# Optimization experiments

Measured on AMD Instinct MI355X. Metric: run time of the kernel, lower is better.

Reference implementation:

```python
import jax, jax.numpy as jnp
import numpy as np

D_MODEL = 1024
H = 16
DK = D_MODEL // H
B, S = 2, 2048
NEG = -1e9


def setup_inputs() -> dict:
    key = jax.random.key(0)
    ks = jax.random.split(key, 7)
    scale = 1.0 / np.sqrt(D_MODEL)
    inp = {
        "q": jax.random.normal(ks[0], (B, S, D_MODEL), jnp.float32),
        "k": jax.random.normal(ks[1], (B, S, D_MODEL), jnp.float32),
        "v": jax.random.normal(ks[2], (B, S, D_MODEL), jnp.float32),
        # causal mask, broadcastable to (B, H, S, S); positions with 0 are masked
        "mask": jnp.tril(jnp.ones((S, S), dtype=bool))[None, None, :, :],
        "w_q": jax.random.normal(ks[3], (D_MODEL, D_MODEL), jnp.float32) * scale,
        "w_k": jax.random.normal(ks[4], (D_MODEL, D_MODEL), jnp.float32) * scale,
        "w_v": jax.random.normal(ks[5], (D_MODEL, D_MODEL), jnp.float32) * scale,
        "w_o": jax.random.normal(ks[6], (D_MODEL, D_MODEL), jnp.float32) * scale,
    }
    return inp


def reference(q, k, v, mask, w_q, w_k, w_v, w_o):
    # Linear projections (nn.Linear with bias=False: x @ W.T)
    query = q @ w_q.T  # (B, S, d_model)
    key_ = k @ w_k.T
    value = v @ w_v.T
    # split heads -> (B, h, S, dk)
    def split(x):
        return x.reshape(x.shape[0], x.shape[1], H, DK).transpose(0, 2, 1, 3)
    qh, kh, vh = split(query), split(key_), split(value)
    # scaled dot-product attention with full score materialization
    scores = jnp.einsum("bhqd,bhkd->bhqk", qh, kh) / jnp.sqrt(jnp.float32(DK))
    scores = jnp.where(mask, scores, NEG)
    attn = jax.nn.softmax(scores, axis=-1)  # (B, h, S, S); dropout p=0.0 -> identity
    out = jnp.einsum("bhqk,bhkd->bhqd", attn, vh)
    # merge heads -> (B, S, d_model)
    out = out.transpose(0, 2, 1, 3).reshape(out.shape[0], -1, H * DK)
    return out @ w_o.T
```

## Files before the change

kernel.cpp:

```cpp
#include <hip/hip_runtime.h>
#include <cstdint>
#include <cstddef>

typedef __bf16 bf16;
typedef __attribute__((ext_vector_type(4))) __bf16 bf16x4;
typedef __attribute__((ext_vector_type(8))) __bf16 bf16x8;
typedef __attribute__((ext_vector_type(4))) float floatx4;
typedef __attribute__((ext_vector_type(4))) short short4v;

#define MFMA16(a, b, c) __builtin_amdgcn_mfma_f32_16x16x32_bf16((a), (b), (c), 0, 0, 0)

__device__ __forceinline__ floatx4 MFMAK16(bf16x4 a, bf16x4 b, floatx4 c) {
#if __has_builtin(__builtin_amdgcn_mfma_f32_16x16x16bf16_1k)
  return __builtin_amdgcn_mfma_f32_16x16x16bf16_1k(
      __builtin_bit_cast(short4v, a), __builtin_bit_cast(short4v, b), c, 0, 0, 0);
#else
  floatx4 d;
  asm("v_mfma_f32_16x16x16_bf16 %0, %1, %2, %3"
      : "=v"(d)
      : "v"(a), "v"(b), "v"(c));
  return d;
#endif
}

constexpr int DMODEL = 1024;
constexpr int NH = 16;
constexpr int DKH = 64;
constexpr int B_ = 2;
constexpr int S_ = 2048;
constexpr int MTOT = B_ * S_;
constexpr float CEXP = 0.125f * 1.44269504f;

__device__ __forceinline__ void load_lds16(const void* g, void* l) {
  __builtin_amdgcn_global_load_lds(
      (const __attribute__((address_space(1))) uint32_t*)g,
      (__attribute__((address_space(3))) uint32_t*)l, 16, 0, 0);
}

__device__ __forceinline__ bf16x8 frag64(const bf16* lds, int row, int p) {
  int s = p ^ (row & 7);
  return *(const bf16x8*)&lds[row * 64 + s * 8];
}
__device__ __forceinline__ bf16x4 frag64h(const bf16* lds, int row, int p, int h) {
  int s = p ^ (row & 7);
  return *(const bf16x4*)&lds[row * 64 + s * 8 + h * 4];
}

__device__ __forceinline__ void stage32_bf16(const bf16* __restrict__ src,
                                             bf16* lds, int wave, int lane,
                                             int ldg) {
#pragma unroll
  for (int i = 0; i < 2; ++i) {
    int cb = (wave * 2 + i) * 64;
    int c = cb + lane;
    int r = c >> 2;
    int s = (c & 3) ^ ((r >> 1) & 3);
    load_lds16(&src[(size_t)r * ldg + s * 8], &lds[cb * 8]);
  }
}
__device__ __forceinline__ bf16x8 frag32_bf16(const bf16* lds, int row,
                                              int quad) {
  int s = quad ^ ((row >> 1) & 3);
  return *(const bf16x8*)&lds[row * 32 + s * 8];
}
__device__ __forceinline__ void stage32_f32(const float* __restrict__ src,
                                            float* lds, int wave, int lane,
                                            int ldg) {
#pragma unroll
  for (int i = 0; i < 4; ++i) {
    int cb = (wave * 4 + i) * 64;
    int c = cb + lane;
    int r = c >> 3;
    int s = (c & 7) ^ (r & 7);
    load_lds16(&src[(size_t)r * ldg + s * 4], &lds[cb * 4]);
  }
}
__device__ __forceinline__ bf16x8 frag32_f32(const float* lds, int row,
                                             int quad) {
  int s1 = (2 * quad) ^ (row & 7);
  int s2 = (2 * quad + 1) ^ (row & 7);
  float4 a = *(const float4*)&lds[row * 32 + s1 * 4];
  float4 b = *(const float4*)&lds[row * 32 + s2 * 4];
  bf16x8 h = {(bf16)a.x, (bf16)a.y, (bf16)a.z, (bf16)a.w,
              (bf16)b.x, (bf16)b.y, (bf16)b.z, (bf16)b.w};
  return h;
}

__global__ __launch_bounds__(256) void convert_kernel(
    const float* __restrict__ q, const float* __restrict__ k,
    const float* __restrict__ v, const float* __restrict__ wq,
    const float* __restrict__ wk, const float* __restrict__ wv,
    const float* __restrict__ wo, bf16* __restrict__ qb, bf16* __restrict__ kb,
    bf16* __restrict__ vb, bf16* __restrict__ wqb, bf16* __restrict__ wkb,
    bf16* __restrict__ wvb, bf16* __restrict__ wob) {
  const float* src;
  bf16* dst;
  size_t n;
  switch (blockIdx.y) {
    case 0: src = q;  dst = qb;  n = (size_t)MTOT * DMODEL; break;
    case 1: src = k;  dst = kb;  n = (size_t)MTOT * DMODEL; break;
    case 2: src = v;  dst = vb;  n = (size_t)MTOT * DMODEL; break;
    case 3: src = wq; dst = wqb; n = (size_t)DMODEL * DMODEL; break;
    case 4: src = wk; dst = wkb; n = (size_t)DMODEL * DMODEL; break;
    case 5: src = wv; dst = wvb; n = (size_t)DMODEL * DMODEL; break;
    default: src = wo; dst = wob; n = (size_t)DMODEL * DMODEL; break;
  }
  size_t idx = ((size_t)blockIdx.x * 256 + threadIdx.x) * 8;
  if (idx >= n) return;
  float4 f0 = *(const float4*)&src[idx];
  float4 f1 = *(const float4*)&src[idx + 4];
  bf16x8 h = {(bf16)f0.x, (bf16)f0.y, (bf16)f0.z, (bf16)f0.w,
              (bf16)f1.x, (bf16)f1.y, (bf16)f1.z, (bf16)f1.w};
  *(bf16x8*)&dst[idx] = h;
}

template <typename TC>
__device__ __forceinline__ void gemm64(const bf16* __restrict__ A,
                                       const bf16* __restrict__ W,
                                       TC* __restrict__ C,
                                       bf16* __restrict__ vt, int K,
                                       int m0, int n0, float ascale) {
  constexpr int N = DMODEL;
  __shared__ alignas(16) bf16 As[128 * 64];
  __shared__ alignas(16) bf16 Bs[128 * 64];

  const int tid = threadIdx.x;
  const int wave = tid >> 6;
  const int lane = tid & 63;
  const int quad = lane >> 4;
  const int l16 = lane & 15;
  const int wm = (wave >> 1) * 64;
  const int wn = (wave & 1) * 64;

  floatx4 acc[4][4] = {};

  for (int k0 = 0; k0 < K; k0 += 64) {
#pragma unroll
    for (int i = 0; i < 4; ++i) {
      int cb = (wave * 4 + i) * 64;
      int c = cb + lane;
      int r = c >> 3;
      int s = (c & 7) ^ (r & 7);
      load_lds16(&A[(size_t)(m0 + r) * K + k0 + s * 8], &As[cb * 8]);
      load_lds16(&W[(size_t)(n0 + r) * K + k0 + s * 8], &Bs[cb * 8]);
    }
    __syncthreads();

#pragma unroll
    for (int kk = 0; kk < 2; ++kk) {
      bf16x8 af[4], bfv[4];
#pragma unroll
      for (int mi = 0; mi < 4; ++mi)
        af[mi] = frag64(As, wm + mi * 16 + l16, kk * 4 + quad);
#pragma unroll
      for (int ni = 0; ni < 4; ++ni)
        bfv[ni] = frag64(Bs, wn + ni * 16 + l16, kk * 4 + quad);
#pragma unroll
      for (int mi = 0; mi < 4; ++mi)
#pragma unroll
        for (int ni = 0; ni < 4; ++ni)
          acc[mi][ni] = MFMA16(af[mi], bfv[ni], acc[mi][ni]);
    }
    __syncthreads();
  }

  if (vt) {
#pragma unroll
    for (int mi = 0; mi < 4; ++mi)
#pragma unroll
      for (int ni = 0; ni < 4; ++ni)
#pragma unroll
        for (int r = 0; r < 4; ++r) {
          int row = m0 + wm + mi * 16 + quad * 4 + r;
          int col = n0 + wn + ni * 16 + l16;
          int bb = row >> 11, s = row & 2047;
          int h = col >> 6, d = col & 63;
          vt[(size_t)((bb * NH + h) * DKH + d) * S_ + s] = (bf16)acc[mi][ni][r];
        }
  } else {
#pragma unroll
    for (int mi = 0; mi < 4; ++mi)
#pragma unroll
      for (int ni = 0; ni < 4; ++ni)
#pragma unroll
        for (int r = 0; r < 4; ++r) {
          int row = m0 + wm + mi * 16 + quad * 4 + r;
          int col = n0 + wn + ni * 16 + l16;
          C[(size_t)row * N + col] = (TC)(acc[mi][ni][r] * ascale);
        }
  }
}

__global__ __launch_bounds__(256, 3) void qkv64_kernel(
    const bf16* __restrict__ q, const bf16* __restrict__ k,
    const bf16* __restrict__ v, const bf16* __restrict__ wq,
    const bf16* __restrict__ wk, const bf16* __restrict__ wv,
    bf16* __restrict__ Q, bf16* __restrict__ K, bf16* __restrict__ Vt) {
  const int bid = blockIdx.x;
  const int xcd = bid & 7;
  const int j = bid >> 3;
  const int n = j & 7;
  const int rowslot = j >> 3;
  const int p = xcd * 12 + rowslot;
  const int z = p >> 5;
  const int y = p & 31;

  const bf16* A = (z == 0) ? q : (z == 1) ? k : v;
  const bf16* W = (z == 0) ? wq : (z == 1) ? wk : wv;
  bf16* C = (z == 0) ? Q : K;
  gemm64<bf16>(A, W, (z == 2) ? nullptr : C, (z == 2) ? Vt : nullptr,
               DMODEL, y * 128, n * 128, (z == 0) ? CEXP : 1.0f);
}

__global__ __launch_bounds__(256) void oproj64_kernel(
    const bf16* __restrict__ A, const bf16* __restrict__ W,
    float* __restrict__ C) {
  constexpr int K = DMODEL;
  constexpr int N = DMODEL;
  __shared__ alignas(16) bf16 As[64 * 64];
  __shared__ alignas(16) bf16 Bs[128 * 64];

  const int bid = blockIdx.x;
  const int xcd = bid & 7;
  const int j = bid >> 3;
  const int n = j & 7;
  const int slot = j >> 3;
  const int mt = xcd * 8 + slot;
  const int m0 = mt * 64;
  const int n0 = n * 128;

  const int tid = threadIdx.x;
  const int wave = tid >> 6;
  const int lane = tid & 63;
  const int quad = lane >> 4;
  const int l16 = lane & 15;
  const int wm = (wave >> 1) * 32;
  const int wn = (wave & 1) * 64;

  floatx4 acc[2][4] = {};

  for (int k0 = 0; k0 < K; k0 += 64) {
#pragma unroll
    for (int i = 0; i < 2; ++i) {
      int cb = (wave * 2 + i) * 64;
      int c = cb + lane;
      int r = c >> 3;
      int s = (c & 7) ^ (r & 7);
      load_lds16(&A[(size_t)(m0 + r) * K + k0 + s * 8], &As[cb * 8]);
    }
#pragma unroll
    for (int i = 0; i < 4; ++i) {
      int cb = (wave * 4 + i) * 64;
      int c = cb + lane;
      int r = c >> 3;
      int s = (c & 7) ^ (r & 7);
      load_lds16(&W[(size_t)(n0 + r) * K + k0 + s * 8], &Bs[cb * 8]);
    }
    __syncthreads();

#pragma unroll
    for (int kk = 0; kk < 2; ++kk) {
      bf16x8 af[2], bfv[4];
#pragma unroll
      for (int mi = 0; mi < 2; ++mi)
        af[mi] = frag64(As, wm + mi * 16 + l16, kk * 4 + quad);
#pragma unroll
      for (int ni = 0; ni < 4; ++ni)
        bfv[ni] = frag64(Bs, wn + ni * 16 + l16, kk * 4 + quad);
#pragma unroll
      for (int mi = 0; mi < 2; ++mi)
#pragma unroll
        for (int ni = 0; ni < 4; ++ni)
          acc[mi][ni] = MFMA16(af[mi], bfv[ni], acc[mi][ni]);
    }
    __syncthreads();
  }

#pragma unroll
  for (int mi = 0; mi < 2; ++mi)
#pragma unroll
    for (int ni = 0; ni < 4; ++ni)
#pragma unroll
      for (int r = 0; r < 4; ++r) {
        int row = m0 + wm + mi * 16 + quad * 4 + r;
        int col = n0 + wn + ni * 16 + l16;
        C[(size_t)row * N + col] = acc[mi][ni][r];
      }
}

template <typename TA, typename TW, typename TC>
__device__ __forceinline__ void gemm_core(const TA* __restrict__ A,
                                          const TW* __restrict__ W,
                                          TC* __restrict__ C,
                                          bf16* __restrict__ vt, int K,
                                          int m0, int n0, float ascale) {
  constexpr int N = DMODEL;
  __shared__ alignas(16) char smem[128 * 32 * (sizeof(TA) + sizeof(TW))];
  TA* As = (TA*)smem;
  TW* Bs = (TW*)(smem + 128 * 32 * sizeof(TA));

  const int tid = threadIdx.x;
  const int wave = tid >> 6;
  const int lane = tid & 63;
  const int quad = lane >> 4;
  const int l16 = lane & 15;
  const int wm = (wave >> 1) * 64;
  const int wn = (wave & 1) * 64;

  floatx4 acc[4][4] = {};

  for (int k0 = 0; k0 < K; k0 += 32) {
    if constexpr (sizeof(TA) == 2)
      stage32_bf16((const bf16*)A + (size_t)m0 * K + k0, (bf16*)As, wave, lane, K);
    else
      stage32_f32((const float*)A + (size_t)m0 * K + k0, (float*)As, wave, lane, K);
    if constexpr (sizeof(TW) == 2)
      stage32_bf16((const bf16*)W + (size_t)n0 * K + k0, (bf16*)Bs, wave, lane, K);
    else
      stage32_f32((const float*)W + (size_t)n0 * K + k0, (float*)Bs, wave, lane, K);
    __syncthreads();

    bf16x8 af[4], bfv[4];
#pragma unroll
    for (int mi = 0; mi < 4; ++mi) {
      if constexpr (sizeof(TA) == 2)
        af[mi] = frag32_bf16((const bf16*)As, wm + mi * 16 + l16, quad);
      else
        af[mi] = frag32_f32((const float*)As, wm + mi * 16 + l16, quad);
    }
#pragma unroll
    for (int ni = 0; ni < 4; ++ni) {
      if constexpr (sizeof(TW) == 2)
        bfv[ni] = frag32_bf16((const bf16*)Bs, wn + ni * 16 + l16, quad);
      else
        bfv[ni] = frag32_f32((const float*)Bs, wn + ni * 16 + l16, quad);
    }
#pragma unroll
    for (int mi = 0; mi < 4; ++mi)
#pragma unroll
      for (int ni = 0; ni < 4; ++ni)
        acc[mi][ni] = MFMA16(af[mi], bfv[ni], acc[mi][ni]);
    __syncthreads();
  }

  if (vt) {
#pragma unroll
    for (int mi = 0; mi < 4; ++mi)
#pragma unroll
      for (int ni = 0; ni < 4; ++ni)
#pragma unroll
        for (int r = 0; r < 4; ++r) {
          int row = m0 + wm + mi * 16 + quad * 4 + r;
          int col = n0 + wn + ni * 16 + l16;
          int bb = row >> 11, s = row & 2047;
          int h = col >> 6, d = col & 63;
          vt[(size_t)((bb * NH + h) * DKH + d) * S_ + s] = (bf16)acc[mi][ni][r];
        }
  } else {
#pragma unroll
    for (int mi = 0; mi < 4; ++mi)
#pragma unroll
      for (int ni = 0; ni < 4; ++ni)
#pragma unroll
        for (int r = 0; r < 4; ++r) {
          int row = m0 + wm + mi * 16 + quad * 4 + r;
          int col = n0 + wn + ni * 16 + l16;
          C[(size_t)row * N + col] = (TC)(acc[mi][ni][r] * ascale);
        }
  }
}

__global__ __launch_bounds__(256) void qkv_f32_kernel(
    const float* __restrict__ q, const float* __restrict__ k,
    const float* __restrict__ v, const float* __restrict__ wq,
    const float* __restrict__ wk, const float* __restrict__ wv,
    bf16* __restrict__ Q, bf16* __restrict__ K, bf16* __restrict__ Vt) {
  const int bid = blockIdx.x;
  const int xcd = bid & 7;
  const int j = bid >> 3;
  const int n = j & 7;
  const int rowslot = j >> 3;
  const int p = xcd * 12 + rowslot;
  const int z = p >> 5;
  const int y = p & 31;
  const float* A = (z == 0) ? q : (z == 1) ? k : v;
  const float* W = (z == 0) ? wq : (z == 1) ? wk : wv;
  bf16* C = (z == 0) ? Q : K;
  gemm_core<float, float, bf16>(A, W, (z == 2) ? nullptr : C,
                                (z == 2) ? Vt : nullptr, DMODEL, y * 128,
                                n * 128, (z == 0) ? CEXP : 1.0f);
}

__global__ __launch_bounds__(256) void oproj_f32_kernel(
    const bf16* __restrict__ A, const float* __restrict__ W,
    float* __restrict__ C) {
  const int bid = blockIdx.x;
  const int xcd = bid & 7;
  const int j = bid >> 3;
  const int n = j & 7;
  const int rowslot = j >> 3;
  const int y = xcd * 4 + rowslot;
  gemm_core<bf16, float, float>(A, W, C, nullptr, DMODEL, y * 128, n * 128,
                                1.0f);
}

__device__ __forceinline__ void stage_kv(const bf16* __restrict__ K,
                                         const bf16* __restrict__ Vt,
                                         bf16* Ks, bf16* Vts, size_t baseQ,
                                         size_t baseV, int kt, int wave,
                                         int lane) {
#pragma unroll
  for (int i = 0; i < 2; ++i) {
    int cb = (wave * 2 + i) * 64;
    int c = cb + lane;
    int r = c >> 3;
    int s = (c & 7) ^ (r & 7);
    load_lds16(&K[baseQ + (size_t)(kt * 64 + r) * DMODEL + s * 8], &Ks[cb * 8]);
    load_lds16(&Vt[baseV + (size_t)r * S_ + kt * 64 + s * 8], &Vts[cb * 8]);
  }
}

template <bool DIAG>
__device__ __forceinline__ void attn_tile(const bf16* Ks, const bf16* Vts,
                                          const bf16x8 qf[2], floatx4 ot[4],
                                          float lp[4], int quad, int l16,
                                          int qb) {
  floatx4 sa[4] = {};
#pragma unroll
  for (int kk = 0; kk < 2; ++kk)
#pragma unroll
    for (int kg = 0; kg < 4; ++kg) {
      bf16x8 ka = frag64(Ks, kg * 16 + l16, kk * 4 + quad);
      sa[kg] = MFMA16(ka, qf[kk], sa[kg]);
    }

  bf16x4 pb[4];
#pragma unroll
  for (int kg = 0; kg < 4; ++kg) {
    float pv[4];
#pragma unroll
    for (int r = 0; r < 4; ++r) {
      float s = sa[kg][r];
      if (DIAG) {
        int key = kg * 16 + quad * 4 + r;
        s = (key > qb) ? -3.0e38f : s;
      }
      float p = __builtin_amdgcn_exp2f(s);
      lp[kg] += p;
      pv[r] = p;
    }
    pb[kg] = bf16x4{(bf16)pv[0], (bf16)pv[1], (bf16)pv[2], (bf16)pv[3]};
  }

#pragma unroll
  for (int kg = 0; kg < 4; ++kg)
#pragma unroll
    for (int di = 0; di < 4; ++di) {
      bf16x4 va = frag64h(Vts, di * 16 + l16, kg * 2 + (quad >> 1), quad & 1);
      ot[di] = MFMAK16(va, pb[kg], ot[di]);
    }
}

__global__ __launch_bounds__(256) void attn7_kernel(const bf16* __restrict__ Q,
                                                    const bf16* __restrict__ K,
                                                    const bf16* __restrict__ Vt,
                                                    bf16* __restrict__ O) {
  __shared__ alignas(16) bf16 Ks[2][64 * 64];
  __shared__ alignas(16) bf16 Vts[2][64 * 64];

  const int tid = threadIdx.x;
  const int wave = tid >> 6;
  const int lane = tid & 63;
  const int quad = lane >> 4;
  const int l16 = lane & 15;

  const int j = blockIdx.x;
  const int bh = j & 31;
  const int pr = j >> 5;
  const int qtL = pr;
  const int qtH = 31 - pr;
  const int h = bh & 15;
  const int b = bh >> 4;
  const size_t baseQ = (size_t)b * S_ * DMODEL + (size_t)h * DKH;
  const size_t baseV = (size_t)bh * DKH * S_;

  bf16x8 qfL[2], qfH[2];
#pragma unroll
  for (int kk = 0; kk < 2; ++kk) {
    qfL[kk] = *(const bf16x8*)&Q[baseQ +
        (size_t)(qtL * 64 + wave * 16 + l16) * DMODEL + kk * 32 + quad * 8];
    qfH[kk] = *(const bf16x8*)&Q[baseQ +
        (size_t)(qtH * 64 + wave * 16 + l16) * DMODEL + kk * 32 + quad * 8];
  }

  floatx4 otL[4] = {}, otH[4] = {};
  float lpL[4] = {}, lpH[4] = {};
  const int qb = wave * 16 + l16;

  stage_kv(K, Vt, Ks[0], Vts[0], baseQ, baseV, 0, wave, lane);
  __syncthreads();

  for (int kt = 0; kt < qtH; ++kt) {
    const int cur = kt & 1;
    stage_kv(K, Vt, Ks[cur ^ 1], Vts[cur ^ 1], baseQ, baseV, kt + 1, wave, lane);

    __builtin_amdgcn_s_setprio(1);
    if (kt < qtL)
      attn_tile<false>(Ks[cur], Vts[cur], qfL, otL, lpL, quad, l16, qb);
    else if (kt == qtL)
      attn_tile<true>(Ks[cur], Vts[cur], qfL, otL, lpL, quad, l16, qb);
    attn_tile<false>(Ks[cur], Vts[cur], qfH, otH, lpH, quad, l16, qb);
    __builtin_amdgcn_s_setprio(0);

    __syncthreads();
  }
  {
    const int cur = qtH & 1;
    attn_tile<true>(Ks[cur], Vts[cur], qfH, otH, lpH, quad, l16, qb);
  }

  float lL = (lpL[0] + lpL[1]) + (lpL[2] + lpL[3]);
  lL += __shfl_xor(lL, 16, 64);
  lL += __shfl_xor(lL, 32, 64);
  float lH = (lpH[0] + lpH[1]) + (lpH[2] + lpH[3]);
  lH += __shfl_xor(lH, 16, 64);
  lH += __shfl_xor(lH, 32, 64);
  const float invL = 1.0f / lL;
  const float invH = 1.0f / lH;

  const size_t orowL = baseQ + (size_t)(qtL * 64 + wave * 16 + l16) * DMODEL;
  const size_t orowH = baseQ + (size_t)(qtH * 64 + wave * 16 + l16) * DMODEL;
#pragma unroll
  for (int di = 0; di < 4; ++di)
#pragma unroll
    for (int r = 0; r < 4; ++r) {
      O[orowL + di * 16 + quad * 4 + r] = (bf16)(otL[di][r] * invL);
      O[orowH + di * 16 + quad * 4 + r] = (bf16)(otH[di][r] * invH);
    }
}

extern "C" void kernel_launch(void* const* d_in, const int* in_sizes, int n_in,
                              void* d_out, int out_size, void* d_ws,
                              size_t ws_size, hipStream_t stream) {
  const float* q = (const float*)d_in[0];
  const float* k = (const float*)d_in[1];
  const float* v = (const float*)d_in[2];
  const float* wq = (const float*)d_in[4];
  const float* wk = (const float*)d_in[5];
  const float* wv = (const float*)d_in[6];
  const float* wo = (const float*)d_in[7];
  float* out = (float*)d_out;

  const size_t MB = 1024 * 1024;
  char* base = (char*)d_ws;
  bf16* Qp = (bf16*)(base);
  bf16* Kp = (bf16*)(base + 8 * MB);
  bf16* VtG = (bf16*)(base + 16 * MB);
  bf16* AO = (bf16*)(base + 24 * MB);

  if (ws_size >= 64 * MB) {
    bf16* qb = (bf16*)(base + 32 * MB);
    bf16* kb = (bf16*)(base + 40 * MB);
    bf16* vb = (bf16*)(base + 48 * MB);
    bf16* wqb = (bf16*)(base + 56 * MB);
    bf16* wkb = (bf16*)(base + 58 * MB);
    bf16* wvb = (bf16*)(base + 60 * MB);
    bf16* wob = (bf16*)(base + 62 * MB);
    convert_kernel<<<dim3(2048, 7), 256, 0, stream>>>(
        q, k, v, wq, wk, wv, wo, qb, kb, vb, wqb, wkb, wvb, wob);
    qkv64_kernel<<<dim3(768), 256, 0, stream>>>(
        qb, kb, vb, wqb, wkb, wvb, Qp, Kp, VtG);
    attn7_kernel<<<dim3(512), 256, 0, stream>>>(Qp, Kp, VtG, AO);
    oproj64_kernel<<<dim3(512), 256, 0, stream>>>(AO, wob, out);
  } else {
    qkv_f32_kernel<<<dim3(768), 256, 0, stream>>>(
        q, k, v, wq, wk, wv, Qp, Kp, VtG);
    attn7_kernel<<<dim3(512), 256, 0, stream>>>(Qp, Kp, VtG, AO);
    oproj_f32_kernel<<<dim3(256), 256, 0, stream>>>(AO, wo, out);
  }
}
```

Measured before the change: 208.2 us.

## Use two waves of 32 query rows with register-cached K/V fragments

The attention kernel now runs 128 threads per block, and each wave handles 32 query rows instead of 16. K and V fragments are loaded from LDS into registers once per key tile and reused across both 16-row query groups, which halves the LDS fragment reads per query row. Each wave now stages more of the K/V tile. The cost is higher register pressure and fewer waves resident per CU, which reduces latency hiding.

```diff
diff --git a/kernel.cpp b/kernel.cpp
--- a/kernel.cpp
+++ b/kernel.cpp
@@ -404,14 +404,14 @@
                                 1.0f);
 }
 
-__device__ __forceinline__ void stage_kv(const bf16* __restrict__ K,
-                                         const bf16* __restrict__ Vt,
-                                         bf16* Ks, bf16* Vts, size_t baseQ,
-                                         size_t baseV, int kt, int wave,
-                                         int lane) {
-#pragma unroll
-  for (int i = 0; i < 2; ++i) {
-    int cb = (wave * 2 + i) * 64;
+__device__ __forceinline__ void stage_kv2(const bf16* __restrict__ K,
+                                          const bf16* __restrict__ Vt,
+                                          bf16* Ks, bf16* Vts, size_t baseQ,
+                                          size_t baseV, int kt, int wave,
+                                          int lane) {
+#pragma unroll
+  for (int i = 0; i < 4; ++i) {
+    int cb = (wave * 4 + i) * 64;
     int c = cb + lane;
     int r = c >> 3;
     int s = (c & 7) ^ (r & 7);
@@ -421,50 +421,51 @@
 }
 
 template <bool DIAG>
-__device__ __forceinline__ void attn_tile(const bf16* Ks, const bf16* Vts,
-                                          const bf16x8 qf[2], floatx4 ot[4],
-                                          float lp[4], int quad, int l16,
-                                          int qb) {
-  floatx4 sa[4] = {};
-#pragma unroll
-  for (int kk = 0; kk < 2; ++kk)
+__device__ __forceinline__ void tile32(const bf16x8 (&ka)[2][4],
+                                       const bf16x4 (&va)[4][4],
+                                       const bf16x8 (&qf)[2][2],
+                                       floatx4 (&ot)[2][4], float (&lp)[2][4],
+                                       int quad, int l16, int qh) {
+#pragma unroll
+  for (int qg = 0; qg < 2; ++qg) {
+    floatx4 sa[4] = {};
+#pragma unroll
+    for (int kk = 0; kk < 2; ++kk)
+#pragma unroll
+      for (int kg = 0; kg < 4; ++kg)
+        sa[kg] = MFMA16(ka[kk][kg], qf[qg][kk], sa[kg]);
+
+    const int qb = qh * 32 + qg * 16 + l16;
+    bf16x4 pb[4];
 #pragma unroll
     for (int kg = 0; kg < 4; ++kg) {
-      bf16x8 ka = frag64(Ks, kg * 16 + l16, kk * 4 + quad);
-      sa[kg] = MFMA16(ka, qf[kk], sa[kg]);
-    }
-
-  bf16x4 pb[4];
-#pragma unroll
-  for (int kg = 0; kg < 4; ++kg) {
-    float pv[4];
-#pragma unroll
-    for (int r = 0; r < 4; ++r) {
-      float s = sa[kg][r];
-      if (DIAG) {
-        int key = kg * 16 + quad * 4 + r;
-        s = (key > qb) ? -3.0e38f : s;
+      float pv[4];
+#pragma unroll
+      for (int r = 0; r < 4; ++r) {
+        float s = sa[kg][r];
+        if (DIAG) {
+          int key = kg * 16 + quad * 4 + r;
+          s = (key > qb) ? -3.0e38f : s;
+        }
+        float p = __builtin_amdgcn_exp2f(s);
+        lp[qg][kg] += p;
+        pv[r] = p;
       }
-      float p = __builtin_amdgcn_exp2f(s);
-      lp[kg] += p;
-      pv[r] = p;
-    }
-    pb[kg] = bf16x4{(bf16)pv[0], (bf16)pv[1], (bf16)pv[2], (bf16)pv[3]};
-  }
-
-#pragma unroll
-  for (int kg = 0; kg < 4; ++kg)
-#pragma unroll
-    for (int di = 0; di < 4; ++di) {
-      bf16x4 va = frag64h(Vts, di * 16 + l16, kg * 2 + (quad >> 1), quad & 1);
-      ot[di] = MFMAK16(va, pb[kg], ot[di]);
-    }
-}
-
-__global__ __launch_bounds__(256) void attn7_kernel(const bf16* __restrict__ Q,
-                                                    const bf16* __restrict__ K,
-                                                    const bf16* __restrict__ Vt,
-                                                    bf16* __restrict__ O) {
+      pb[kg] = bf16x4{(bf16)pv[0], (bf16)pv[1], (bf16)pv[2], (bf16)pv[3]};
+    }
+
+#pragma unroll
+    for (int kg = 0; kg < 4; ++kg)
+#pragma unroll
+      for (int di = 0; di < 4; ++di)
+        ot[qg][di] = MFMAK16(va[kg][di], pb[kg], ot[qg][di]);
+  }
+}
+
+__global__ __launch_bounds__(128, 1) void attn9_kernel(const bf16* __restrict__ Q,
+                                                       const bf16* __restrict__ K,
+                                                       const bf16* __restrict__ Vt,
+                                                       bf16* __restrict__ O) {
   __shared__ alignas(16) bf16 Ks[2][64 * 64];
   __shared__ alignas(16) bf16 Vts[2][64 * 64];
 
@@ -473,6 +474,7 @@
   const int lane = tid & 63;
   const int quad = lane >> 4;
   const int l16 = lane & 15;
+  const int qh = wave;
 
   const int j = blockIdx.x;
   const int bh = j & 31;
@@ -484,59 +486,91 @@
   const size_t baseQ = (size_t)b * S_ * DMODEL + (size_t)h * DKH;
   const size_t baseV = (size_t)bh * DKH * S_;
 
-  bf16x8 qfL[2], qfH[2];
-#pragma unroll
-  for (int kk = 0; kk < 2; ++kk) {
-    qfL[kk] = *(const bf16x8*)&Q[baseQ +
-        (size_t)(qtL * 64 + wave * 16 + l16) * DMODEL + kk * 32 + quad * 8];
-    qfH[kk] = *(const bf16x8*)&Q[baseQ +
-        (size_t)(qtH * 64 + wave * 16 + l16) * DMODEL + kk * 32 + quad * 8];
-  }
-
-  floatx4 otL[4] = {}, otH[4] = {};
-  float lpL[4] = {}, lpH[4] = {};
-  const int qb = wave * 16 + l16;
-
-  stage_kv(K, Vt, Ks[0], Vts[0], baseQ, baseV, 0, wave, lane);
+  bf16x8 qf[2][2][2];
+#pragma unroll
+  for (int t = 0; t < 2; ++t) {
+    const int qt = t ? qtH : qtL;
+#pragma unroll
+    for (int qg = 0; qg < 2; ++qg)
+#pragma unroll
+      for (int kk = 0; kk < 2; ++kk)
+        qf[t][qg][kk] = *(const bf16x8*)&Q[baseQ +
+            (size_t)(qt * 64 + qh * 32 + qg * 16 + l16) * DMODEL + kk * 32 +
+            quad * 8];
+  }
+
+  floatx4 ot[2][2][4] = {};
+  float lp[2][2][4] = {};
+  
+  stage_kv2(K, Vt, Ks[0], Vts[0], baseQ, baseV, 0, wave, lane);
   __syncthreads();
 
   for (int kt = 0; kt < qtH; ++kt) {
     const int cur = kt & 1;
-    stage_kv(K, Vt, Ks[cur ^ 1], Vts[cur ^ 1], baseQ, baseV, kt + 1, wave, lane);
+    stage_kv2(K, Vt, Ks[cur ^ 1], Vts[cur ^ 1], baseQ, baseV, kt + 1, wave, lane);
 
     __builtin_amdgcn_s_setprio(1);
-    if (kt < qtL)
-      attn_tile<false>(Ks[cur], Vts[cur], qfL, otL, lpL, quad, l16, qb);
-    else if (kt == qtL)
-      attn_tile<true>(Ks[cur], Vts[cur], qfL, otL, lpL, quad, l16, qb);
-    attn_tile<false>(Ks[cur], Vts[cur], qfH, otH, lpH, quad, l16, qb);
+    bf16x8 ka[2][4];
+    bf16x4 va[4][4];
+#pragma unroll
+    for (int kk = 0; kk < 2; ++kk)
+#pragma unroll
+      for (int kg = 0; kg < 4; ++kg)
+        ka[kk][kg] = frag64(Ks[cur], kg * 16 + l16, kk * 4 + quad);
+#pragma unroll
+    for (int kg = 0; kg < 4; ++kg)
+#pragma unroll
+      for (int di = 0; di < 4; ++di)
+        va[kg][di] = frag64h(Vts[cur], di * 16 + l16, kg * 2 + (quad >> 1), quad & 1);
+
+    if (kt < qtL) {
+      tile32<false>(ka, va, qf[0], ot[0], lp[0], quad, l16, qh);
+      tile32<false>(ka, va, qf[1], ot[1], lp[1], quad, l16, qh);
+    } else if (kt == qtL) {
+      tile32<true>(ka, va, qf[0], ot[0], lp[0], quad, l16, qh);
+      tile32<false>(ka, va, qf[1], ot[1], lp[1], quad, l16, qh);
+    } else {
+      tile32<false>(ka, va, qf[1], ot[1], lp[1], quad, l16, qh);
+    }
     __builtin_amdgcn_s_setprio(0);
 
     __syncthreads();
   }
   {
     const int cur = qtH & 1;
-    attn_tile<true>(Ks[cur], Vts[cur], qfH, otH, lpH, quad, l16, qb);
-  }
-
-  float lL = (lpL[0] + lpL[1]) + (lpL[2] + lpL[3]);
-  lL += __shfl_xor(lL, 16, 64);
-  lL += __shfl_xor(lL, 32, 64);
-  float lH = (lpH[0] + lpH[1]) + (lpH[2] + lpH[3]);
-  lH += __shfl_xor(lH, 16, 64);
-  lH += __shfl_xor(lH, 32, 64);
-  const float invL = 1.0f / lL;
-  const float invH = 1.0f / lH;
-
-  const size_t orowL = baseQ + (size_t)(qtL * 64 + wave * 16 + l16) * DMODEL;
-  const size_t orowH = baseQ + (size_t)(qtH * 64 + wave * 16 + l16) * DMODEL;
-#pragma unroll
-  for (int di = 0; di < 4; ++di)
-#pragma unroll
-    for (int r = 0; r < 4; ++r) {
-      O[orowL + di * 16 + quad * 4 + r] = (bf16)(otL[di][r] * invL);
-      O[orowH + di * 16 + quad * 4 + r] = (bf16)(otH[di][r] * invH);
-    }
+    bf16x8 ka[2][4];
+    bf16x4 va[4][4];
+#pragma unroll
+    for (int kk = 0; kk < 2; ++kk)
+#pragma unroll
+      for (int kg = 0; kg < 4; ++kg)
+        ka[kk][kg] = frag64(Ks[cur], kg * 16 + l16, kk * 4 + quad);
+#pragma unroll
+    for (int kg = 0; kg < 4; ++kg)
+#pragma unroll
+      for (int di = 0; di < 4; ++di)
+        va[kg][di] = frag64h(Vts[cur], di * 16 + l16, kg * 2 + (quad >> 1), quad & 1);
+    tile32<true>(ka, va, qf[1], ot[1], lp[1], quad, l16, qh);
+  }
+
+#pragma unroll
+  for (int t = 0; t < 2; ++t) {
+    const int qt = t ? qtH : qtL;
+#pragma unroll
+    for (int qg = 0; qg < 2; ++qg) {
+      float l = (lp[t][qg][0] + lp[t][qg][1]) + (lp[t][qg][2] + lp[t][qg][3]);
+      l += __shfl_xor(l, 16, 64);
+      l += __shfl_xor(l, 32, 64);
+      const float inv = 1.0f / l;
+      const size_t orow = baseQ +
+          (size_t)(qt * 64 + qh * 32 + qg * 16 + l16) * DMODEL;
+#pragma unroll
+      for (int di = 0; di < 4; ++di)
+#pragma unroll
+        for (int r = 0; r < 4; ++r)
+          O[orow + di * 16 + quad * 4 + r] = (bf16)(ot[t][qg][di][r] * inv);
+    }
+  }
 }
 
 extern "C" void kernel_launch(void* const* d_in, const int* in_sizes, int n_in,
@@ -570,12 +604,12 @@
         q, k, v, wq, wk, wv, wo, qb, kb, vb, wqb, wkb, wvb, wob);
     qkv64_kernel<<<dim3(768), 256, 0, stream>>>(
         qb, kb, vb, wqb, wkb, wvb, Qp, Kp, VtG);
-    attn7_kernel<<<dim3(512), 256, 0, stream>>>(Qp, Kp, VtG, AO);
+    attn9_kernel<<<dim3(512), 128, 0, stream>>>(Qp, Kp, VtG, AO);
     oproj64_kernel<<<dim3(512), 256, 0, stream>>>(AO, wob, out);
   } else {
     qkv_f32_kernel<<<dim3(768), 256, 0, stream>>>(
         q, k, v, wq, wk, wv, Qp, Kp, VtG);
-    attn7_kernel<<<dim3(512), 256, 0, stream>>>(Qp, Kp, VtG, AO);
+    attn9_kernel<<<dim3(512), 128, 0, stream>>>(Qp, Kp, VtG, AO);
     oproj_f32_kernel<<<dim3(256), 256, 0, stream>>>(AO, wo, out);
   }
 }
```

Result: slower. 214.5 us (+3.0%).
